# Kernel optimization log

Measured on AMD Instinct MI355X. Metric: run time of the kernel, lower is better.

The kernel has to match this reference:

```python
import jax, jax.numpy as jnp
import numpy as np

B, C, S, D = 4, 16, 512, 512
H = 8
HD = D // H
FFN = 2048
MAX_WL = 10000.0
ROPE_PCT = 0.5
EPS = 1e-5


def setup_inputs() -> dict:
    key = jax.random.key(0)
    ks = jax.random.split(key, 8)
    w = lambda k, shape: jax.random.normal(k, shape, jnp.float32) * 0.02
    return {
        "x": jax.random.normal(ks[0], (B, C, S, D), jnp.float32),
        "Wq": w(ks[1], (D, D)), "bq": jnp.zeros((D,), jnp.float32),
        "Wk": w(ks[2], (D, D)), "bk": jnp.zeros((D,), jnp.float32),
        "Wv": w(ks[3], (D, D)), "bv": jnp.zeros((D,), jnp.float32),
        "Wo": w(ks[4], (D, D)), "bo": jnp.zeros((D,), jnp.float32),
        "ln1_g": jnp.ones((D,), jnp.float32), "ln1_b": jnp.zeros((D,), jnp.float32),
        "ln3_g": jnp.ones((D,), jnp.float32), "ln3_b": jnp.zeros((D,), jnp.float32),
        "W1": w(ks[5], (D, FFN)), "b1": jnp.zeros((FFN,), jnp.float32),
        "W2": w(ks[6], (FFN, D)), "b2": jnp.zeros((D,), jnp.float32),
    }


def _layernorm(x, g, b):
    mu = jnp.mean(x, axis=-1, keepdims=True)
    var = jnp.mean((x - mu) ** 2, axis=-1, keepdims=True)
    return (x - mu) * jax.lax.rsqrt(var + EPS) * g + b


def _p_rope(x, pos):
    # partial rotary: rotate first ROPE_PCT fraction of rotation angles, pass rest through
    half = HD // 2
    rope_angles = int(ROPE_PCT * HD) // 2  # 16 for HD=64, pct=0.5
    exps = (2.0 / HD) * jnp.arange(rope_angles, dtype=jnp.float32)
    timescale = MAX_WL ** exps
    timescale = jnp.concatenate([timescale, jnp.full((half - rope_angles,), jnp.inf, jnp.float32)])
    ang = pos[:, None] / timescale[None, :]  # (S, half); inf timescale -> angle 0 -> identity
    sin, cos = jnp.sin(ang), jnp.cos(ang)
    x1, x2 = x[..., :half], x[..., half:]
    return jnp.concatenate([x1 * cos - x2 * sin, x2 * cos + x1 * sin], axis=-1)


def _forward(x, Wq, bq, Wk, bk, Wv, bv, Wo, bo, ln1_g, ln1_b, ln3_g, ln3_b, W1, b1, W2, b2):
    h = x.reshape(B * C, S, D)
    # --- temporal self-attention (pre-norm) ---
    hn = _layernorm(h, ln1_g, ln1_b)
    scaling = HD ** -0.5
    q = (hn @ Wq + bq) * scaling
    k = hn @ Wk + bk
    v = hn @ Wv + bv
    split = lambda t: t.reshape(B * C, S, H, HD).transpose(0, 2, 1, 3)  # (BC,H,S,HD)
    q, k, v = split(q), split(k), split(v)
    pos = jnp.arange(S, dtype=jnp.float32)
    q = _p_rope(q, pos)
    k = _p_rope(k, pos)
    attn = jax.nn.softmax(jnp.einsum('bhqd,bhkd->bhqk', q, k), axis=-1)
    o = jnp.einsum('bhqk,bhkd->bhqd', attn, v)
    o = o.transpose(0, 2, 1, 3).reshape(B * C, S, D) @ Wo + bo
    h = h + o
    # --- feed-forward (pre-norm) ---
    hn = _layernorm(h, ln3_g, ln3_b)
    ff = jax.nn.gelu(hn @ W1 + b1, approximate=False) @ W2 + b2
    h = h + ff
    return h.reshape(B, C, S, D)


def reference(x, Wq, bq, Wk, bk, Wv, bv, Wo, bo, ln1_g, ln1_b, ln3_g, ln3_b, W1, b1, W2, b2):
    return _forward(x, Wq, bq, Wk, bk, Wv, bv, Wo, bo, ln1_g, ln1_b, ln3_g, ln3_b, W1, b1, W2, b2)
```

## Files before the change

### kernel.cpp

```cpp
#include <hip/hip_runtime.h>
#include <math.h>

typedef unsigned short u16;
typedef __attribute__((ext_vector_type(8))) short bf16x8;
typedef __attribute__((ext_vector_type(4))) float f32x4;

#define MFMA16(a, b, c) __builtin_amdgcn_mfma_f32_16x16x32_bf16((a), (b), (c), 0, 0, 0)

__device__ __forceinline__ u16 f2bf(float f) {
    union { float f; unsigned u; } v; v.f = f;
    unsigned u = v.u;
    unsigned r = (u + 0x7FFFu + ((u >> 16) & 1u)) >> 16;
    return (u16)r;
}

__device__ __forceinline__ unsigned pack_bf16(float lo, float hi) {
    union { float f; unsigned u; } a, b; a.f = lo; b.f = hi;
    return __builtin_amdgcn_perm(b.u + 0x8000u, a.u + 0x8000u, 0x07060302u);
}

__device__ __forceinline__ float fexp2(float x) {
#if __has_builtin(__builtin_amdgcn_exp2f)
    return __builtin_amdgcn_exp2f(x);
#else
    return __expf(x * 0.6931471805599453f);
#endif
}

__device__ __forceinline__ float frcp(float x) {
#if __has_builtin(__builtin_amdgcn_rcpf)
    return __builtin_amdgcn_rcpf(x);
#else
    return 1.0f / x;
#endif
}

__device__ __forceinline__ float fgelu(float v) {
    float x2 = v * v;
    float u = v * (0.7978845608028654f + 0.035677408136300125f * x2);
    return v * frcp(1.0f + fexp2(-2.8853900817779268f * u));
}

__device__ __forceinline__ void gl_lds16(const u16* g, u16* l) {
    __builtin_amdgcn_global_load_lds(
        (const __attribute__((address_space(1))) unsigned*)g,
        (__attribute__((address_space(3))) unsigned*)l, 16, 0, 0);
}

__global__ __launch_bounds__(256) void transpose_cvt_all(
    const float* __restrict__ Wq, const float* __restrict__ Wk,
    const float* __restrict__ Wv, const float* __restrict__ Wo,
    const float* __restrict__ W1, const float* __restrict__ W2,
    u16* __restrict__ wqt, u16* __restrict__ wkt, u16* __restrict__ wvt,
    u16* __restrict__ wot, u16* __restrict__ w1t, u16* __restrict__ w2t)
{
    __shared__ float tile[64][65];
    int fb = blockIdx.x;
    const float* src; u16* dst; int K, N, bx, by;
    if (fb < 256) {
        int w = fb >> 6, b = fb & 63;
        src = (w == 0) ? Wq : (w == 1) ? Wk : (w == 2) ? Wv : Wo;
        dst = (w == 0) ? wqt : (w == 1) ? wkt : (w == 2) ? wvt : wot;
        K = 512; N = 512; bx = b & 7; by = b >> 3;
    } else if (fb < 512) {
        int b = fb - 256; src = W1; dst = w1t; K = 512; N = 2048; bx = b & 31; by = b >> 5;
    } else {
        int b = fb - 512; src = W2; dst = w2t; K = 2048; N = 512; bx = b & 7; by = b >> 3;
    }
    int n0 = bx * 64, k0 = by * 64;
    int tx = threadIdx.x & 63, ty = threadIdx.x >> 6;
    #pragma unroll
    for (int i = ty; i < 64; i += 4)
        tile[i][tx] = src[(size_t)(k0 + i) * N + n0 + tx];
    __syncthreads();
    #pragma unroll
    for (int i = ty; i < 64; i += 4)
        dst[(size_t)(n0 + i) * K + k0 + tx] = f2bf(tile[tx][i]);
}

__global__ __launch_bounds__(256) void ln_kernel(const float* __restrict__ in,
                                                 u16* __restrict__ out,
                                                 const float* __restrict__ g,
                                                 const float* __restrict__ b) {
    int row = blockIdx.x;
    const float* rp = in + (size_t)row * 512;
    int t = threadIdx.x;
    float2 v = *(const float2*)(rp + t * 2);
    float s = v.x + v.y;
    float sq = v.x * v.x + v.y * v.y;
    #pragma unroll
    for (int off = 32; off > 0; off >>= 1) {
        s  += __shfl_down(s, off, 64);
        sq += __shfl_down(sq, off, 64);
    }
    __shared__ float red[8];
    __shared__ float stat[2];
    int wid = t >> 6;
    if ((t & 63) == 0) { red[wid] = s; red[wid + 4] = sq; }
    __syncthreads();
    if (t == 0) {
        float S = red[0] + red[1] + red[2] + red[3];
        float Q = red[4] + red[5] + red[6] + red[7];
        float mu = S * (1.0f / 512.0f);
        float var = Q * (1.0f / 512.0f) - mu * mu;
        stat[0] = mu;
        stat[1] = rsqrtf(var + 1e-5f);
    }
    __syncthreads();
    float mu = stat[0], inv = stat[1];
    int c = t * 2;
    float2 gv = *(const float2*)(g + c);
    float2 bv = *(const float2*)(b + c);
    ushort2 ov;
    ov.x = f2bf((v.x - mu) * inv * gv.x + bv.x);
    ov.y = f2bf((v.y - mu) * inv * gv.y + bv.y);
    *(ushort2*)(out + (size_t)row * 512 + c) = ov;
}


#define FENCE() asm volatile("" ::: "memory")
#define BARF()  do { FENCE(); __builtin_amdgcn_s_barrier(); FENCE(); } while (0)
#define LGKM0() asm volatile("s_waitcnt lgkmcnt(0)" ::: "memory")
#define VM0()   asm volatile("s_waitcnt vmcnt(0)" ::: "memory")
#define PRIO1() __builtin_amdgcn_s_setprio(1)
#define PRIO0() __builtin_amdgcn_s_setprio(0)

__device__ __forceinline__ bf16x8 ldfrag(const u16* __restrict__ base, int R, int ko, int lq) {
    int o = (ko + lq * 8) ^ ((R & 7) * 8);
    return *(const bf16x8*)(base + R * 64 + o);
}

__device__ __forceinline__ void gemm256_core(
    const u16* __restrict__ A, const u16* __restrict__ Bt, int K,
    int m0, int n0, int t, u16* __restrict__ smem, f32x4 (&acc)[8][4])
{
    const int NS = K >> 6;
    const int wid = t >> 6, lane = t & 63;
    const int lm = lane & 15, lq = lane >> 4;
    const int wm_ = wid >> 2;
    const int wn_ = wid & 3;
    const int wbh = wn_ >> 1;
    const int wbr = (wn_ & 1) * 64;

    auto reg = [&](int buf, int ab, int half) -> u16* {
        return smem + (((buf << 1) | ab) * 2 + half) * 8192;
    };

    const int r0 = t >> 3;
    const int csw = ((t & 7) * 8) ^ ((r0 & 7) * 8);
    const u16* gA = A + (size_t)(m0 + r0) * K + csw;
    const u16* gB = Bt + (size_t)(n0 + r0) * K + csw;
    const size_t pK64 = (size_t)64 * K;
    const size_t hK128 = (size_t)128 * K;

    auto stA = [&](int u, int hf) {
        if (u >= NS) return;
        u16* d = reg(u & 1, 0, hf) + t * 8;
        const u16* s = gA + (size_t)(u * 64) + (hf ? hK128 : (size_t)0);
        gl_lds16(s, d);
        gl_lds16(s + pK64, d + 4096);
    };
    auto stB = [&](int u, int hf) {
        if (u >= NS) return;
        u16* d = reg(u & 1, 1, hf) + t * 8;
        const u16* s = gB + (size_t)(u * 64) + (hf ? hK128 : (size_t)0);
        gl_lds16(s, d);
        gl_lds16(s + pK64, d + 4096);
    };

    #pragma unroll
    for (int i = 0; i < 8; ++i)
        #pragma unroll
        for (int j = 0; j < 4; ++j) acc[i][j] = (f32x4){0.f, 0.f, 0.f, 0.f};

    stB(0, 0); stB(0, 1); stA(0, 0); stA(0, 1);
    VM0();
    BARF();

    for (int s = 0; s < NS; ++s) {
        const u16* As = reg(s & 1, 0, wm_);
        const u16* Bs = reg(s & 1, 1, wbh);
        stA(s + 1, 0);
        stA(s + 1, 1);
        stB(s + 1, 0);
        stB(s + 1, 1);
        bf16x8 aF[4], bF[4][2];
        #pragma unroll
        for (int i = 0; i < 4; ++i) aF[i] = ldfrag(As, i * 16 + lm, 0, lq);
        #pragma unroll
        for (int j = 0; j < 4; ++j) bF[j][0] = ldfrag(Bs, wbr + j * 16 + lm, 0, lq);
        PRIO1();
        #pragma unroll
        for (int i = 0; i < 4; ++i)
            #pragma unroll
            for (int j = 0; j < 4; ++j)
                acc[i][j] = MFMA16(aF[i], bF[j][0], acc[i][j]);
        PRIO0();
        #pragma unroll
        for (int i = 0; i < 4; ++i) aF[i] = ldfrag(As, i * 16 + lm, 32, lq);
        #pragma unroll
        for (int j = 0; j < 4; ++j) bF[j][1] = ldfrag(Bs, wbr + j * 16 + lm, 32, lq);
        PRIO1();
        #pragma unroll
        for (int i = 0; i < 4; ++i)
            #pragma unroll
            for (int j = 0; j < 4; ++j)
                acc[i][j] = MFMA16(aF[i], bF[j][1], acc[i][j]);
        PRIO0();
        #pragma unroll
        for (int i = 0; i < 4; ++i) aF[i] = ldfrag(As, 64 + i * 16 + lm, 0, lq);
        PRIO1();
        #pragma unroll
        for (int i = 0; i < 4; ++i)
            #pragma unroll
            for (int j = 0; j < 4; ++j)
                acc[4 + i][j] = MFMA16(aF[i], bF[j][0], acc[4 + i][j]);
        PRIO0();
        #pragma unroll
        for (int i = 0; i < 4; ++i) aF[i] = ldfrag(As, 64 + i * 16 + lm, 32, lq);
        PRIO1();
        #pragma unroll
        for (int i = 0; i < 4; ++i)
            #pragma unroll
            for (int j = 0; j < 4; ++j)
                acc[4 + i][j] = MFMA16(aF[i], bF[j][1], acc[4 + i][j]);
        PRIO0();
        LGKM0();
        VM0();
        BARF();
    }
}

__global__ __launch_bounds__(512) void qkv256_kernel(
    const u16* __restrict__ A,
    const u16* __restrict__ wqt, const u16* __restrict__ wkt, const u16* __restrict__ wvt,
    const float* __restrict__ bqp, const float* __restrict__ bkp, const float* __restrict__ bvp,
    u16* __restrict__ qb, u16* __restrict__ kb, u16* __restrict__ vb, float sclq)
{
    __shared__ u16 smem[65536];
    int flat = blockIdx.x;
    int xcd = flat & 7, slot = flat >> 3;
    int g = xcd * 96 + slot;
    int mt = g / 6, nt = g % 6;
    int mode = nt >> 1;
    int m0 = mt * 256, nb0 = (nt & 1) * 256;
    const u16* Bt = (mode == 0) ? wqt : (mode == 1) ? wkt : wvt;
    const float* bias = (mode == 0) ? bqp : (mode == 1) ? bkp : bvp;
    u16* outp = (mode == 0) ? qb : (mode == 1) ? kb : vb;

    int t = threadIdx.x;
    f32x4 acc[8][4];
    gemm256_core(A, Bt, 512, m0, nb0, t, smem, acc);

    int wid = t >> 6, lane = t & 63, lm = lane & 15, lq = lane >> 4;
    int rowb = m0 + (wid >> 2) * 128;
    int colb = nb0 + (wid & 3) * 64;

    if (mode < 2) {
        float bv0 = bias[colb + 0 * 16 + lm];
        float bv1 = bias[colb + 1 * 16 + lm];
        float bv2 = bias[colb + 2 * 16 + lm];
        float bv3 = bias[colb + 3 * 16 + lm];
        float its = __expf((float)lm * -0.28782313662425572f);
        float scl = (mode == 0) ? sclq : 1.f;
        #pragma unroll
        for (int i = 0; i < 8; ++i) {
            #pragma unroll
            for (int r = 0; r < 4; ++r) {
                int gm = rowb + i * 16 + lq * 4 + r;
                int s = gm & 511;
                float ang = (float)s * its;
                float sn = __sinf(ang), cs = __cosf(ang);
                float x1 = acc[i][0][r] + bv0;
                float x2 = acc[i][2][r] + bv2;
                float y0 = (x1 * cs - x2 * sn) * scl;
                float y2 = (x2 * cs + x1 * sn) * scl;
                float y1 = (acc[i][1][r] + bv1) * scl;
                float y3 = (acc[i][3][r] + bv3) * scl;
                size_t base = ((size_t)(gm >> 9)) * 262144 + (size_t)(colb >> 6) * 32768
                            + (size_t)s * 64 + lm;
                outp[base +  0] = f2bf(y0);
                outp[base + 16] = f2bf(y1);
                outp[base + 32] = f2bf(y2);
                outp[base + 48] = f2bf(y3);
            }
        }
    } else {
        #pragma unroll
        for (int i = 0; i < 8; ++i)
            #pragma unroll
            for (int j = 0; j < 4; ++j) {
                int gn = colb + j * 16 + lm;
                float bvv = bias[gn];
                #pragma unroll
                for (int r = 0; r < 4; ++r) {
                    int gm = rowb + i * 16 + lq * 4 + r;
                    float v = acc[i][j][r] + bvv;
                    size_t idx = ((size_t)(gm >> 9)) * 262144 + (size_t)(gn >> 6) * 32768
                               + (size_t)(gn & 63) * 512 + (gm & 511);
                    outp[idx] = f2bf(v);
                }
            }
    }
}

template<int MODE>
__global__ __launch_bounds__(512) void gemm256_kernel(
    const u16* __restrict__ A, const u16* __restrict__ Bt,
    const float* __restrict__ bias, const float* __restrict__ res,
    void* __restrict__ outp, int M, int N, int K)
{
    __shared__ u16 smem[65536];
    int flat = blockIdx.x;
    int nbt = N >> 8;
    int nwg = (M >> 8) * nbt;
    int xcd = flat & 7, slot = flat >> 3;
    int g = xcd * (nwg >> 3) + slot;
    int mt = g / nbt, nt = g % nbt;
    int m0 = mt * 256, n0 = nt * 256;

    int t = threadIdx.x;
    f32x4 acc[8][4];
    gemm256_core(A, Bt, K, m0, n0, t, smem, acc);

    int wid = t >> 6, lane = t & 63, lm = lane & 15, lq = lane >> 4;
    int rowb = m0 + (wid >> 2) * 128, colb = n0 + (wid & 3) * 64;
    #pragma unroll
    for (int i = 0; i < 8; ++i)
        #pragma unroll
        for (int j = 0; j < 4; ++j) {
            int gn = colb + j * 16 + lm;
            float bv = bias[gn];
            #pragma unroll
            for (int r = 0; r < 4; ++r) {
                int gm = rowb + i * 16 + lq * 4 + r;
                float v = acc[i][j][r] + bv;
                if (MODE == 3) {
                    size_t idx = (size_t)gm * N + gn;
                    ((float*)outp)[idx] = v + res[idx];
                } else {
                    ((u16*)outp)[(size_t)gm * N + gn] = f2bf(fgelu(v));
                }
            }
        }
}

__global__ __launch_bounds__(256, 3) void attn_kernel(
    const u16* __restrict__ q, const u16* __restrict__ k,
    const u16* __restrict__ vt, u16* __restrict__ o)
{
    int flat = blockIdx.y * gridDim.x + blockIdx.x;
    int xcd = flat & 7, slot = flat >> 3;
    int nh = xcd * 64 + (slot >> 1);
    int qt = slot & 1;
    const u16* Qb = q + (size_t)nh * 32768 + (size_t)qt * 16384;
    const u16* Kb = k + (size_t)nh * 32768;
    const u16* Vb = vt + (size_t)nh * 32768;
    __shared__ u16 sKV[2][2][4096];
    __shared__ u16 lP[4][16][72];
    int t = threadIdx.x, wid = t >> 6, lane = t & 63, lm = lane & 15, lq = lane >> 4;

    auto stKV = [&](int kt, int buf) {
        if (kt >= 8) return;
        #pragma unroll
        for (int p = 0; p < 2; ++p) {
            int idx = p * 256 + t;
            int row = idx >> 3;
            int c = ((idx & 7) * 8) ^ ((row & 7) * 8);
            gl_lds16(Kb + (size_t)(kt * 64 + row) * 64 + c, &sKV[buf][0][idx * 8]);
            gl_lds16(Vb + (size_t)row * 512 + kt * 64 + c, &sKV[buf][1][idx * 8]);
        }
    };
    auto ldsw = [&](const u16* base, int row, int cu16) -> bf16x8 {
        return *(const bf16x8*)&base[row * 64 + (cu16 ^ ((row & 7) * 8))];
    };

    bf16x8 bq[4][2];
    #pragma unroll
    for (int sub = 0; sub < 4; ++sub) {
        const u16* qr = Qb + (size_t)(sub * 64 + wid * 16 + lm) * 64;
        bq[sub][0] = *(const bf16x8*)(qr + lq * 8);
        bq[sub][1] = *(const bf16x8*)(qr + 32 + lq * 8);
    }

    const f32x4 zero = {0.f, 0.f, 0.f, 0.f};
    f32x4 Oacc[4][4];
    float mo[4], l[4];
    #pragma unroll
    for (int s = 0; s < 4; ++s) {
        mo[s] = -INFINITY; l[s] = 0.f;
        #pragma unroll
        for (int d = 0; d < 4; ++d) Oacc[s][d] = zero;
    }

    stKV(0, 0);
    VM0(); BARF();

    for (int kt = 0; kt < 8; ++kt) {
        int buf = kt & 1;
        stKV(kt + 1, buf ^ 1);
        const u16* Kl = sKV[buf][0];
        const u16* Vl = sKV[buf][1];
        bf16x8 aK[4][2];
        #pragma unroll
        for (int i = 0; i < 4; ++i) {
            aK[i][0] = ldsw(Kl, i * 16 + lm, lq * 8);
            aK[i][1] = ldsw(Kl, i * 16 + lm, 32 + lq * 8);
        }
        #pragma unroll
        for (int sub = 0; sub < 4; ++sub) {
            f32x4 sc[4];
            #pragma unroll
            for (int i = 0; i < 4; ++i) {
                f32x4 z = MFMA16(aK[i][0], bq[sub][0], zero);
                sc[i] = MFMA16(aK[i][1], bq[sub][1], z);
            }
            float mx = sc[0][0];
            #pragma unroll
            for (int i = 0; i < 4; ++i)
                #pragma unroll
                for (int r = 0; r < 4; ++r) mx = fmaxf(mx, sc[i][r]);
            mx = fmaxf(mx, __shfl_xor(mx, 16, 64));
            mx = fmaxf(mx, __shfl_xor(mx, 32, 64));
            if (!__all(mx <= mo[sub] + 8.0f)) {
                float mn = fmaxf(mo[sub], mx);
                float al = fexp2(mo[sub] - mn);
                l[sub] *= al;
                #pragma unroll
                for (int dn = 0; dn < 4; ++dn) Oacc[sub][dn] *= al;
                mo[sub] = mn;
            }
            float mc = mo[sub];
            float sum = 0.f;
            #pragma unroll
            for (int i = 0; i < 4; ++i)
                #pragma unroll
                for (int r = 0; r < 4; ++r) {
                    float p = fexp2(sc[i][r] - mc);
                    sc[i][r] = p;
                    sum += p;
                }
            sum += __shfl_xor(sum, 16, 64);
            sum += __shfl_xor(sum, 32, 64);
            l[sub] += sum;
            #pragma unroll
            for (int i = 0; i < 4; ++i) {
                uint2 w2;
                w2.x = pack_bf16(sc[i][0], sc[i][1]);
                w2.y = pack_bf16(sc[i][2], sc[i][3]);
                *(uint2*)&lP[wid][lm][i * 16 + lq * 4] = w2;
            }
            bf16x8 bp0 = *(const bf16x8*)&lP[wid][lm][lq * 8];
            bf16x8 bp1 = *(const bf16x8*)&lP[wid][lm][32 + lq * 8];
            #pragma unroll
            for (int dn = 0; dn < 4; ++dn) {
                bf16x8 v0 = ldsw(Vl, dn * 16 + lm, lq * 8);
                bf16x8 v1 = ldsw(Vl, dn * 16 + lm, 32 + lq * 8);
                Oacc[sub][dn] = MFMA16(v0, bp0, Oacc[sub][dn]);
                Oacc[sub][dn] = MFMA16(v1, bp1, Oacc[sub][dn]);
            }
        }
        LGKM0(); VM0(); BARF();
    }
    int bc = nh >> 3, h = nh & 7;
    #pragma unroll
    for (int sub = 0; sub < 4; ++sub) {
        float inv = 1.f / l[sub];
        size_t orow = ((size_t)(bc * 512 + qt * 256 + sub * 64 + wid * 16 + lm)) * 512 + h * 64;
        #pragma unroll
        for (int dn = 0; dn < 4; ++dn) {
            uint2 w2;
            w2.x = pack_bf16(Oacc[sub][dn][0] * inv, Oacc[sub][dn][1] * inv);
            w2.y = pack_bf16(Oacc[sub][dn][2] * inv, Oacc[sub][dn][3] * inv);
            *(uint2*)(o + orow + dn * 16 + lq * 4) = w2;
        }
    }
}

extern "C" void kernel_launch(void* const* d_in, const int* in_sizes, int n_in,
                              void* d_out, int out_size, void* d_ws, size_t ws_size,
                              hipStream_t stream) {
    const float* x    = (const float*)d_in[0];
    const float* Wq   = (const float*)d_in[1];
    const float* bq   = (const float*)d_in[2];
    const float* Wk   = (const float*)d_in[3];
    const float* bk   = (const float*)d_in[4];
    const float* Wv   = (const float*)d_in[5];
    const float* bv   = (const float*)d_in[6];
    const float* Wo   = (const float*)d_in[7];
    const float* bo   = (const float*)d_in[8];
    const float* ln1g = (const float*)d_in[9];
    const float* ln1b = (const float*)d_in[10];
    const float* ln3g = (const float*)d_in[11];
    const float* ln3b = (const float*)d_in[12];
    const float* W1   = (const float*)d_in[13];
    const float* b1   = (const float*)d_in[14];
    const float* W2   = (const float*)d_in[15];
    const float* b2   = (const float*)d_in[16];

    char* ws = (char*)d_ws;
    u16*  hn  = (u16*)(ws + 0ull);
    u16*  qb  = (u16*)(ws + 33554432ull);
    u16*  kb  = (u16*)(ws + 67108864ull);
    u16*  vb  = (u16*)(ws + 100663296ull);
    u16*  ob  = (u16*)(ws + 134217728ull);
    u16*  ffa = (u16*)(ws + 33554432ull);
    float* h1 = (float*)(ws + 167772160ull);
    u16*  wqt = (u16*)(ws + 234881024ull);
    u16*  wkt = (u16*)(ws + 235405312ull);
    u16*  wvt = (u16*)(ws + 235929600ull);
    u16*  wot = (u16*)(ws + 236453888ull);
    u16*  w1t = (u16*)(ws + 236978176ull);
    u16*  w2t = (u16*)(ws + 239075328ull);

    dim3 blk(256);
    transpose_cvt_all<<<768, blk, 0, stream>>>(Wq, Wk, Wv, Wo, W1, W2,
                                               wqt, wkt, wvt, wot, w1t, w2t);

    ln_kernel<<<32768, blk, 0, stream>>>(x, hn, ln1g, ln1b);

    qkv256_kernel<<<768, dim3(512), 0, stream>>>(hn, wqt, wkt, wvt, bq, bk, bv,
                                                 qb, kb, vb,
                                                 0.125f * 1.4426950408889634f);

    attn_kernel<<<dim3(2, 512), blk, 0, stream>>>(qb, kb, vb, ob);

    gemm256_kernel<3><<<256, dim3(512), 0, stream>>>(ob, wot, bo, x, h1,
                                                     32768, 512, 512);

    ln_kernel<<<32768, blk, 0, stream>>>(h1, hn, ln3g, ln3b);

    gemm256_kernel<4><<<1024, dim3(512), 0, stream>>>(hn, w1t, b1, nullptr, ffa,
                                                      32768, 2048, 512);
    gemm256_kernel<3><<<256, dim3(512), 0, stream>>>(ffa, w2t, b2, h1,
                                                     (float*)d_out, 32768, 512, 2048);
}
```

Before: 570.5 us.

## Use 16 waves per 256x256 GEMM tile with 64x64 per-wave subtiles

Switches the GEMM workgroups from 512 to 1024 threads, giving each of 16 waves a 64x64 output subtile instead of 128x64. This halves the accumulator registers per thread, and each thread now issues one global-to-LDS load per slab instead of two. It aims to get more waves in flight to hide latency. The trade-off is more LDS fragment reads per MFMA and heavier barrier synchronisation across 16 waves.

```diff
diff --git a/kernel.cpp b/kernel.cpp
--- a/kernel.cpp
+++ b/kernel.cpp
@@ -132,15 +132,15 @@
 
 __device__ __forceinline__ void gemm256_core(
     const u16* __restrict__ A, const u16* __restrict__ Bt, int K,
-    int m0, int n0, int t, u16* __restrict__ smem, f32x4 (&acc)[8][4])
+    int m0, int n0, int t, u16* __restrict__ smem, f32x4 (&acc)[4][4])
 {
     const int NS = K >> 6;
     const int wid = t >> 6, lane = t & 63;
     const int lm = lane & 15, lq = lane >> 4;
     const int wm_ = wid >> 2;
     const int wn_ = wid & 3;
-    const int wbh = wn_ >> 1;
-    const int wbr = (wn_ & 1) * 64;
+    const int ar = (wm_ & 1) * 64;
+    const int br = (wn_ & 1) * 64;
 
     auto reg = [&](int buf, int ab, int half) -> u16* {
         return smem + (((buf << 1) | ab) * 2 + half) * 8192;
@@ -150,80 +150,55 @@
     const int csw = ((t & 7) * 8) ^ ((r0 & 7) * 8);
     const u16* gA = A + (size_t)(m0 + r0) * K + csw;
     const u16* gB = Bt + (size_t)(n0 + r0) * K + csw;
-    const size_t pK64 = (size_t)64 * K;
     const size_t hK128 = (size_t)128 * K;
 
     auto stA = [&](int u, int hf) {
         if (u >= NS) return;
-        u16* d = reg(u & 1, 0, hf) + t * 8;
-        const u16* s = gA + (size_t)(u * 64) + (hf ? hK128 : (size_t)0);
-        gl_lds16(s, d);
-        gl_lds16(s + pK64, d + 4096);
+        gl_lds16(gA + (size_t)(u * 64) + (hf ? hK128 : (size_t)0),
+                 reg(u & 1, 0, hf) + t * 8);
     };
     auto stB = [&](int u, int hf) {
         if (u >= NS) return;
-        u16* d = reg(u & 1, 1, hf) + t * 8;
-        const u16* s = gB + (size_t)(u * 64) + (hf ? hK128 : (size_t)0);
-        gl_lds16(s, d);
-        gl_lds16(s + pK64, d + 4096);
+        gl_lds16(gB + (size_t)(u * 64) + (hf ? hK128 : (size_t)0),
+                 reg(u & 1, 1, hf) + t * 8);
     };
 
     #pragma unroll
-    for (int i = 0; i < 8; ++i)
+    for (int i = 0; i < 4; ++i)
         #pragma unroll
         for (int j = 0; j < 4; ++j) acc[i][j] = (f32x4){0.f, 0.f, 0.f, 0.f};
 
-    stB(0, 0); stB(0, 1); stA(0, 0); stA(0, 1);
+    stA(0, 0); stA(0, 1); stB(0, 0); stB(0, 1);
     VM0();
     BARF();
 
     for (int s = 0; s < NS; ++s) {
-        const u16* As = reg(s & 1, 0, wm_);
-        const u16* Bs = reg(s & 1, 1, wbh);
-        stA(s + 1, 0);
-        stA(s + 1, 1);
-        stB(s + 1, 0);
-        stB(s + 1, 1);
-        bf16x8 aF[4], bF[4][2];
-        #pragma unroll
-        for (int i = 0; i < 4; ++i) aF[i] = ldfrag(As, i * 16 + lm, 0, lq);
-        #pragma unroll
-        for (int j = 0; j < 4; ++j) bF[j][0] = ldfrag(Bs, wbr + j * 16 + lm, 0, lq);
+        const u16* As = reg(s & 1, 0, wm_ >> 1);
+        const u16* Bs = reg(s & 1, 1, wn_ >> 1);
+        stA(s + 1, 0); stA(s + 1, 1);
+        stB(s + 1, 0); stB(s + 1, 1);
+        bf16x8 aF[4], bF[4];
+        #pragma unroll
+        for (int i = 0; i < 4; ++i) aF[i] = ldfrag(As, ar + i * 16 + lm, 0, lq);
+        #pragma unroll
+        for (int j = 0; j < 4; ++j) bF[j] = ldfrag(Bs, br + j * 16 + lm, 0, lq);
         PRIO1();
         #pragma unroll
         for (int i = 0; i < 4; ++i)
             #pragma unroll
             for (int j = 0; j < 4; ++j)
-                acc[i][j] = MFMA16(aF[i], bF[j][0], acc[i][j]);
+                acc[i][j] = MFMA16(aF[i], bF[j], acc[i][j]);
         PRIO0();
         #pragma unroll
-        for (int i = 0; i < 4; ++i) aF[i] = ldfrag(As, i * 16 + lm, 32, lq);
-        #pragma unroll
-        for (int j = 0; j < 4; ++j) bF[j][1] = ldfrag(Bs, wbr + j * 16 + lm, 32, lq);
+        for (int i = 0; i < 4; ++i) aF[i] = ldfrag(As, ar + i * 16 + lm, 32, lq);
+        #pragma unroll
+        for (int j = 0; j < 4; ++j) bF[j] = ldfrag(Bs, br + j * 16 + lm, 32, lq);
         PRIO1();
         #pragma unroll
         for (int i = 0; i < 4; ++i)
             #pragma unroll
             for (int j = 0; j < 4; ++j)
-                acc[i][j] = MFMA16(aF[i], bF[j][1], acc[i][j]);
-        PRIO0();
-        #pragma unroll
-        for (int i = 0; i < 4; ++i) aF[i] = ldfrag(As, 64 + i * 16 + lm, 0, lq);
-        PRIO1();
-        #pragma unroll
-        for (int i = 0; i < 4; ++i)
-            #pragma unroll
-            for (int j = 0; j < 4; ++j)
-                acc[4 + i][j] = MFMA16(aF[i], bF[j][0], acc[4 + i][j]);
-        PRIO0();
-        #pragma unroll
-        for (int i = 0; i < 4; ++i) aF[i] = ldfrag(As, 64 + i * 16 + lm, 32, lq);
-        PRIO1();
-        #pragma unroll
-        for (int i = 0; i < 4; ++i)
-            #pragma unroll
-            for (int j = 0; j < 4; ++j)
-                acc[4 + i][j] = MFMA16(aF[i], bF[j][1], acc[4 + i][j]);
+                acc[i][j] = MFMA16(aF[i], bF[j], acc[i][j]);
         PRIO0();
         LGKM0();
         VM0();
@@ -231,7 +206,7 @@
     }
 }
 
-__global__ __launch_bounds__(512) void qkv256_kernel(
+__global__ __launch_bounds__(1024) void qkv256_kernel(
     const u16* __restrict__ A,
     const u16* __restrict__ wqt, const u16* __restrict__ wkt, const u16* __restrict__ wvt,
     const float* __restrict__ bqp, const float* __restrict__ bkp, const float* __restrict__ bvp,
@@ -249,11 +224,11 @@
     u16* outp = (mode == 0) ? qb : (mode == 1) ? kb : vb;
 
     int t = threadIdx.x;
-    f32x4 acc[8][4];
+    f32x4 acc[4][4];
     gemm256_core(A, Bt, 512, m0, nb0, t, smem, acc);
 
     int wid = t >> 6, lane = t & 63, lm = lane & 15, lq = lane >> 4;
-    int rowb = m0 + (wid >> 2) * 128;
+    int rowb = m0 + (wid >> 2) * 64;
     int colb = nb0 + (wid & 3) * 64;
 
     if (mode < 2) {
@@ -264,7 +239,7 @@
         float its = __expf((float)lm * -0.28782313662425572f);
         float scl = (mode == 0) ? sclq : 1.f;
         #pragma unroll
-        for (int i = 0; i < 8; ++i) {
+        for (int i = 0; i < 4; ++i) {
             #pragma unroll
             for (int r = 0; r < 4; ++r) {
                 int gm = rowb + i * 16 + lq * 4 + r;
@@ -287,7 +262,7 @@
         }
     } else {
         #pragma unroll
-        for (int i = 0; i < 8; ++i)
+        for (int i = 0; i < 4; ++i)
             #pragma unroll
             for (int j = 0; j < 4; ++j) {
                 int gn = colb + j * 16 + lm;
@@ -305,7 +280,7 @@
 }
 
 template<int MODE>
-__global__ __launch_bounds__(512) void gemm256_kernel(
+__global__ __launch_bounds__(1024) void gemm256_kernel(
     const u16* __restrict__ A, const u16* __restrict__ Bt,
     const float* __restrict__ bias, const float* __restrict__ res,
     void* __restrict__ outp, int M, int N, int K)
@@ -320,13 +295,13 @@
     int m0 = mt * 256, n0 = nt * 256;
 
     int t = threadIdx.x;
-    f32x4 acc[8][4];
+    f32x4 acc[4][4];
     gemm256_core(A, Bt, K, m0, n0, t, smem, acc);
 
     int wid = t >> 6, lane = t & 63, lm = lane & 15, lq = lane >> 4;
-    int rowb = m0 + (wid >> 2) * 128, colb = n0 + (wid & 3) * 64;
-    #pragma unroll
-    for (int i = 0; i < 8; ++i)
+    int rowb = m0 + (wid >> 2) * 64, colb = n0 + (wid & 3) * 64;
+    #pragma unroll
+    for (int i = 0; i < 4; ++i)
         #pragma unroll
         for (int j = 0; j < 4; ++j) {
             int gn = colb + j * 16 + lm;
@@ -519,19 +494,19 @@
 
     ln_kernel<<<32768, blk, 0, stream>>>(x, hn, ln1g, ln1b);
 
-    qkv256_kernel<<<768, dim3(512), 0, stream>>>(hn, wqt, wkt, wvt, bq, bk, bv,
-                                                 qb, kb, vb,
-                                                 0.125f * 1.4426950408889634f);
+    qkv256_kernel<<<768, dim3(1024), 0, stream>>>(hn, wqt, wkt, wvt, bq, bk, bv,
+                                                  qb, kb, vb,
+                                                  0.125f * 1.4426950408889634f);
 
     attn_kernel<<<dim3(2, 512), blk, 0, stream>>>(qb, kb, vb, ob);
 
-    gemm256_kernel<3><<<256, dim3(512), 0, stream>>>(ob, wot, bo, x, h1,
-                                                     32768, 512, 512);
+    gemm256_kernel<3><<<256, dim3(1024), 0, stream>>>(ob, wot, bo, x, h1,
+                                                      32768, 512, 512);
 
     ln_kernel<<<32768, blk, 0, stream>>>(h1, hn, ln3g, ln3b);
 
-    gemm256_kernel<4><<<1024, dim3(512), 0, stream>>>(hn, w1t, b1, nullptr, ffa,
-                                                      32768, 2048, 512);
-    gemm256_kernel<3><<<256, dim3(512), 0, stream>>>(ffa, w2t, b2, h1,
-                                                     (float*)d_out, 32768, 512, 2048);
-}
+    gemm256_kernel<4><<<1024, dim3(1024), 0, stream>>>(hn, w1t, b1, nullptr, ffa,
+                                                       32768, 2048, 512);
+    gemm256_kernel<3><<<256, dim3(1024), 0, stream>>>(ffa, w2t, b2, h1,
+                                                      (float*)d_out, 32768, 512, 2048);
+}
```

After: 569.5 us. No clear change (-0.2%).
